# Kernel optimization log

Measured on AMD Instinct MI355X. Metric: run time of the kernel, lower is better.

The kernel has to match this reference:

```python
import jax, jax.numpy as jnp
import numpy as np

B, T = 128, 64          # batch, episode length
OB, AC, L, H = 32, 8, 128, 256  # ob_dim, ac_dim, latent_dim, mlp hidden
N_SUB = 4               # fixed Dopri5 substeps per interval (replaces adaptive PID controller)


def setup_inputs() -> dict:
    key = jax.random.key(0)
    ks = jax.random.split(key, 12)
    g = lambda k, shape, fan: jax.random.normal(k, shape, jnp.float32) / np.sqrt(fan)
    return {
        "ob": jax.random.normal(ks[0], (B, OB), jnp.float32),
        "acs": jax.random.normal(ks[1], (B, T, AC), jnp.float32),
        # strictly increasing timestamps (cumsum of uniform increments)
        "times": jnp.cumsum(jax.random.uniform(ks[2], (B, T), jnp.float32, 0.02, 0.1), axis=1),
        # ob encoder MLP (OB -> H -> L), relu hidden, identity out
        "We0": g(ks[3], (H, OB), OB), "be0": jnp.zeros((H,), jnp.float32),
        "We1": g(ks[4], (L, H), H), "be1": jnp.zeros((L,), jnp.float32),
        # latent dynamics MLP (L -> H -> H -> L)
        "Wd0": g(ks[5], (H, L), L), "bd0": jnp.zeros((H,), jnp.float32),
        "Wd1": g(ks[6], (H, H), H), "bd1": jnp.zeros((H,), jnp.float32),
        "Wd2": g(ks[7], (L, H), H), "bd2": jnp.zeros((L,), jnp.float32),
        # ob decoder MLP (L -> H -> OB)
        "Wo0": g(ks[8], (H, L), L), "bo0": jnp.zeros((H,), jnp.float32),
        "Wo1": g(ks[9], (OB, H), H), "bo1": jnp.zeros((OB,), jnp.float32),
        # GRU cell (input=AC, hidden=L), equinox layout: gates [r, z, n]
        "Wih": g(ks[10], (3 * L, AC), AC), "Whh": g(ks[11], (3 * L, L), L),
        "bih": jnp.zeros((3 * L,), jnp.float32), "bn": jnp.zeros((L,), jnp.float32),
    }


def reference(ob, acs, times, We0, be0, We1, be1, Wd0, bd0, Wd1, bd1, Wd2, bd2,
              Wo0, bo0, Wo1, bo1, Wih, Whh, bih, bn):
    def f(y):  # dynamics MLP on batched latent (B, L) -> (B, L)
        h1 = jax.nn.relu(y @ Wd0.T + bd0)
        h2 = jax.nn.relu(h1 @ Wd1.T + bd1)
        return h2 @ Wd2.T + bd2

    def gru(x, h):  # equinox GRUCell math, batched
        ir, iz, inn = jnp.split(x @ Wih.T + bih, 3, axis=-1)
        hr, hz, hn = jnp.split(h @ Whh.T, 3, axis=-1)
        r = jax.nn.sigmoid(ir + hr)
        z = jax.nn.sigmoid(iz + hz)
        n = jnp.tanh(inn + r * (hn + bn))
        return (1.0 - z) * n + z * h

    def dopri5_step(y, h):  # one Dopri5 (RK45) step, h: (B, 1) per-sample step size
        k1 = f(y)
        k2 = f(y + h * (0.2 * k1))
        k3 = f(y + h * (3/40 * k1 + 9/40 * k2))
        k4 = f(y + h * (44/45 * k1 - 56/15 * k2 + 32/9 * k3))
        k5 = f(y + h * (19372/6561 * k1 - 25360/2187 * k2 + 64448/6561 * k3 - 212/729 * k4))
        k6 = f(y + h * (9017/3168 * k1 - 355/33 * k2 + 46732/5247 * k3 + 49/176 * k4 - 5103/18656 * k5))
        return y + h * (35/384 * k1 + 500/1113 * k3 + 125/192 * k4 - 2187/6784 * k5 + 11/84 * k6)

    def integrate(y, dt):  # integrate latent ODE from 0 to dt with N_SUB fixed Dopri5 steps
        h = (dt / N_SUB)[:, None]
        return jax.lax.fori_loop(0, N_SUB, lambda i, yy: dopri5_step(yy, h), y)

    # encode first observation, consume first action
    latent0 = jax.nn.relu(ob @ We0.T + be0) @ We1.T + be1  # (B, L)
    latent0 = gru(acs[:, 0], latent0)

    dts = jnp.diff(times, axis=1)  # (B, T-1)

    def step(latent, xs):
        ac, dt = xs
        latent = integrate(latent, dt)
        latent = gru(ac, latent)
        return latent, latent

    xs = (jnp.swapaxes(acs[:, 1:], 0, 1), dts.T)  # time-major for scan
    _, lat_seq = jax.lax.scan(step, latent0, xs)  # (T-1, B, L)

    latents = jnp.concatenate([latent0[None], lat_seq], axis=0)  # (T, B, L)
    latents = jnp.swapaxes(latents, 0, 1)  # (B, T, L)

    h1 = jax.nn.relu(latents @ Wo0.T + bo0)
    return h1 @ Wo1.T + bo1  # (B, T, OB)
```

## Files before the change

### kernel.cpp

```cpp
#include <hip/hip_runtime.h>
#include <stdint.h>

#define NBATCH 128
#define NT     64
#define OBD    32
#define ACD    8
#define LDIM   128
#define HDIM   256

typedef _Float16 h2 __attribute__((ext_vector_type(2)));
typedef float    f4 __attribute__((ext_vector_type(4)));

#if defined(__has_builtin)
#  if __has_builtin(__builtin_amdgcn_fdot2)
#    define HAVE_FDOT2 1
#  endif
#endif

__device__ __forceinline__ float dot2f(h2 a, h2 b, float c) {
#ifdef HAVE_FDOT2
  return __builtin_amdgcn_fdot2(a, b, c, false);
#else
  return c + (float)a[0] * (float)b[0] + (float)a[1] * (float)b[1];
#endif
}

__device__ __forceinline__ h2 pkh(float a, float b) {
  h2 r; r[0] = (_Float16)a; r[1] = (_Float16)b; return r;
}

__device__ __forceinline__ h2 bch(float x) { return __builtin_bit_cast(h2, x); }
__device__ __forceinline__ float fch(h2 x) { return __builtin_bit_cast(float, x); }

__device__ __forceinline__ float sigmf(float x) { return 1.0f / (1.0f + expf(-x)); }

#define DOT4(W, I, Q) \
    a0 = dot2f(W[4*(I)+0], bch(Q.x), a0); \
    a1 = dot2f(W[4*(I)+1], bch(Q.y), a1); \
    a2 = dot2f(W[4*(I)+2], bch(Q.z), a2); \
    a3 = dot2f(W[4*(I)+3], bch(Q.w), a3);

#define PI(i) ((i) + (((i) >> 5) << 2))
#define PA(i) ((i) + (((i) >> 6) << 2))
#define PB(i) ((i) + (((i) >> 5) << 2))

__global__ void prep_w1(const float* __restrict__ Wd1, f4* __restrict__ ws4) {
  int idx = blockIdx.x * blockDim.x + threadIdx.x;
  int j  = idx >> 9;
  int tt = idx & 511;
  const float* src = Wd1 + (tt >> 1) * HDIM + (tt & 1) * 128 + j * 8;
  f4 c;
  c.x = fch(pkh(src[0], src[1]));
  c.y = fch(pkh(src[2], src[3]));
  c.z = fch(pkh(src[4], src[5]));
  c.w = fch(pkh(src[6], src[7]));
  ws4[j * 512 + tt] = c;
}

__global__ __attribute__((amdgpu_waves_per_eu(2, 2))) __launch_bounds__(512)
void ode_rnn_kernel(const float* __restrict__ ob,   const float* __restrict__ acs,
                    const float* __restrict__ times,
                    const float* __restrict__ We0,  const float* __restrict__ be0,
                    const float* __restrict__ We1,  const float* __restrict__ be1,
                    const float* __restrict__ Wd0,  const float* __restrict__ bd0,
                    const float* __restrict__ bd1,
                    const float* __restrict__ Wd2,  const float* __restrict__ bd2,
                    const float* __restrict__ Wo0,  const float* __restrict__ bo0,
                    const float* __restrict__ Wo1,  const float* __restrict__ bo1,
                    const float* __restrict__ Wih,  const float* __restrict__ Whh,
                    const float* __restrict__ bih,  const float* __restrict__ bn,
                    const f4* __restrict__ ws4,
                    float* __restrict__ out)
{
  const int t    = threadIdx.x;
  const int b    = blockIdx.x;
  const int p    = t >> 1;
  const int sub  = t & 1;
  const int r    = t >> 2;
  const int ksub = t & 3;

  __shared__ __align__(16) float s_lat[LDIM];
  __shared__ __align__(16) float s_gz[LDIM];
  __shared__ __align__(16) float s_gin[LDIM];
  __shared__ __align__(16) float s_ghn[LDIM];
  __shared__ __align__(16) float s_tmp[HDIM];
  __shared__ __align__(16) float s_obs[OBD];
  __shared__ __align__(16) float s_times[NT];
  __shared__ __align__(16) float s_acs[NT * ACD];
  __shared__ __align__(16) h2    s_in16[68];
  __shared__ __align__(16) h2    s_a16[132];
  __shared__ __align__(16) h2    s_b16[140];

  h2 w0[32], w2[32];
  {
    const float2* pp = (const float2*)(Wd0 + p * LDIM + sub * 64);
#pragma unroll
    for (int i = 0; i < 32; ++i) { float2 v = pp[i]; w0[i] = pkh(v.x, v.y); }
  }
  {
    const float2* pp = (const float2*)(Wd2 + r * HDIM + ksub * 64);
#pragma unroll
    for (int i = 0; i < 32; ++i) { float2 v = pp[i]; w2[i] = pkh(v.x, v.y); }
  }
  const f4* wsb = ws4 + t;

  const float bb0 = bd0[p];
  const float bb1 = bd1[p];
  const float bb2 = bd2[r];
  const float rb0 = bo0[p];
  const float gA  = (t < 3 * LDIM) ? bih[t] : 0.0f;
  const float bnr = (t < LDIM) ? bn[t] : 0.0f;

  float latr = 0.0f;

  auto substep = [&](float hs) {
    float k0 = 0, k1 = 0, k2 = 0, k3 = 0, k4 = 0;
#pragma unroll
    for (int s = 0; s < 6; ++s) {
      float a0, a1, a2, a3, v;
      f4 y0 = wsb[0 * 512], y1 = wsb[1 * 512];
      f4 y2 = wsb[2 * 512], y3 = wsb[3 * 512];
      a0 = a1 = a2 = a3 = 0.0f;
      {
        const f4* src = ((const f4*)s_in16) + sub * 9;
#pragma unroll
        for (int i = 0; i < 8; ++i) { f4 q = src[i]; DOT4(w0, i, q) }
      }
      v = (a0 + a1) + (a2 + a3);
      v += __shfl_xor(v, 1);
      v = fmaxf(v + bb0, 0.0f);
      { float ov = __shfl_xor(v, 2); if ((t & 3) == 0) s_a16[PA(t >> 2)] = pkh(v, ov); }
      __syncthreads();
      a0 = a1 = a2 = a3 = 0.0f;
      {
        const f4* act = ((const f4*)s_a16) + sub * 17;
        f4 q;
#define SDOT(WV, J) q = act[J]; \
        a0 = dot2f(bch(WV.x), bch(q.x), a0); \
        a1 = dot2f(bch(WV.y), bch(q.y), a1); \
        a2 = dot2f(bch(WV.z), bch(q.z), a2); \
        a3 = dot2f(bch(WV.w), bch(q.w), a3);
        f4 y4 = wsb[4 * 512],  y5 = wsb[5 * 512];
        SDOT(y0, 0)  SDOT(y1, 1)
        f4 y6 = wsb[6 * 512],  y7 = wsb[7 * 512];
        SDOT(y2, 2)  SDOT(y3, 3)
        f4 y8 = wsb[8 * 512],  y9 = wsb[9 * 512];
        SDOT(y4, 4)  SDOT(y5, 5)
        f4 y10 = wsb[10 * 512], y11 = wsb[11 * 512];
        SDOT(y6, 6)  SDOT(y7, 7)
        f4 y12 = wsb[12 * 512], y13 = wsb[13 * 512];
        SDOT(y8, 8)  SDOT(y9, 9)
        f4 y14 = wsb[14 * 512], y15 = wsb[15 * 512];
        SDOT(y10, 10) SDOT(y11, 11)
        SDOT(y12, 12) SDOT(y13, 13)
        SDOT(y14, 14) SDOT(y15, 15)
#undef SDOT
      }
      v = (a0 + a1) + (a2 + a3);
      v += __shfl_xor(v, 1);
      v = fmaxf(v + bb1, 0.0f);
      { float ov = __shfl_xor(v, 2); if ((t & 3) == 0) s_b16[PB(t >> 2)] = pkh(v, ov); }
      __syncthreads();
      a0 = a1 = a2 = a3 = 0.0f;
      {
        const f4* src = ((const f4*)s_b16) + ksub * 9;
#pragma unroll
        for (int i = 0; i < 8; ++i) { f4 q = src[i]; DOT4(w2, i, q) }
      }
      v = (a0 + a1) + (a2 + a3);
      v += __shfl_xor(v, 1);
      v += __shfl_xor(v, 2);
      float kv = v + bb2;
      float z;
      if (s == 0) {
        k0 = kv; z = latr + hs * (0.2f * kv);
      } else if (s == 1) {
        k1 = kv; z = latr + hs * ((3.0f/40.0f)*k0 + (9.0f/40.0f)*kv);
      } else if (s == 2) {
        k2 = kv; z = latr + hs * ((44.0f/45.0f)*k0 - (56.0f/15.0f)*k1
                                + (32.0f/9.0f)*kv);
      } else if (s == 3) {
        k3 = kv; z = latr + hs * ((19372.0f/6561.0f)*k0 - (25360.0f/2187.0f)*k1
                                + (64448.0f/6561.0f)*k2 - (212.0f/729.0f)*kv);
      } else if (s == 4) {
        k4 = kv; z = latr + hs * ((9017.0f/3168.0f)*k0 - (355.0f/33.0f)*k1
                                + (46732.0f/5247.0f)*k2 + (49.0f/176.0f)*k3
                                - (5103.0f/18656.0f)*kv);
      } else {
        z = latr + hs * ((35.0f/384.0f)*k0 + (500.0f/1113.0f)*k2
                       + (125.0f/192.0f)*k3 - (2187.0f/6784.0f)*k4
                       + (11.0f/84.0f)*kv);
        latr = z;
      }
      { float ov = __shfl_xor(z, 4); if ((t & 7) == 0) s_in16[PI(t >> 3)] = pkh(z, ov); }
      if (s == 5 && ksub == 0) s_lat[r] = z;
      __syncthreads();
    }
  };

  auto gru = [&](int ts) {
    __syncthreads();
    float vi = gA, vh = 0.0f;
    if (t < 3 * LDIM) {
      const float* xa = s_acs + ts * ACD;
      const f4* wiv = (const f4*)(Wih + t * ACD);
      f4 wa = wiv[0], wb = wiv[1];
      vi += wa.x*xa[0] + wa.y*xa[1] + wa.z*xa[2] + wa.w*xa[3]
          + wb.x*xa[4] + wb.y*xa[5] + wb.z*xa[6] + wb.w*xa[7];
      const f4* wh = (const f4*)(Whh + t * LDIM);
      const f4* xl = (const f4*)s_lat;
#pragma unroll
      for (int k2 = 0; k2 < LDIM / 4; ++k2) {
        f4 w = wh[k2], x = xl[k2];
        vh += w.x*x.x + w.y*x.y + w.z*x.z + w.w*x.w;
      }
    }
    if (t >= LDIM && t < 2 * LDIM)          s_gz[t - LDIM] = vi + vh;
    else if (t >= 2 * LDIM && t < 3 * LDIM) { s_gin[t - 2*LDIM] = vi; s_ghn[t - 2*LDIM] = vh; }
    __syncthreads();
    if (t < LDIM) {
      float rg = sigmf(vi + vh);
      float zg = sigmf(s_gz[t]);
      float ng = tanhf(s_gin[t] + rg * (s_ghn[t] + bnr));
      float y  = (1.0f - zg) * ng + zg * s_lat[t];
      s_lat[t] = y;
      float ov = __shfl_xor(y, 1);
      if (!(t & 1)) s_in16[PI(t >> 1)] = pkh(y, ov);
    }
  };

  auto decode = [&](int ts) {
    __syncthreads();
    latr = s_lat[r];
    float acc = 0.0f;
    {
      const f4* wr = (const f4*)(Wo0 + p * LDIM + sub * 64);
      const f4* xl = ((const f4*)s_lat) + sub * 16;
#pragma unroll
      for (int k2 = 0; k2 < 16; ++k2) {
        f4 w = wr[k2], x = xl[k2];
        acc += w.x*x.x + w.y*x.y + w.z*x.z + w.w*x.w;
      }
    }
    acc += __shfl_xor(acc, 1);
    acc = fmaxf(acc + rb0, 0.0f);
    { float ov = __shfl_xor(acc, 2); if ((t & 3) == 0) s_a16[PA(t >> 2)] = pkh(acc, ov); }
    __syncthreads();
    const int o  = t >> 4;
    const int sl = t & 15;
    float v2 = 0.0f;
    {
      const f4* wr = (const f4*)(Wo1 + o * HDIM + sl * 16);
      const h2* xs = s_a16 + sl * 8 + ((sl >> 3) << 2);
#pragma unroll
      for (int i = 0; i < 4; ++i) {
        f4 w = wr[i];
        h2 xa = xs[2*i], xb = xs[2*i+1];
        v2 += w.x*(float)xa[0] + w.y*(float)xa[1]
            + w.z*(float)xb[0] + w.w*(float)xb[1];
      }
    }
    v2 += __shfl_xor(v2, 1);
    v2 += __shfl_xor(v2, 2);
    v2 += __shfl_xor(v2, 4);
    v2 += __shfl_xor(v2, 8);
    if (sl == 0) out[((size_t)b * NT + ts) * OBD + o] = v2 + bo1[o];
    __syncthreads();
  };

  if (t < OBD) s_obs[t] = ob[b * OBD + t];
  if (t < NT)  s_times[t] = times[b * NT + t];
  s_acs[t] = acs[(size_t)b * NT * ACD + t];
  __syncthreads();
  if (t < HDIM) {
    float acc = be0[t];
    const float* wr = We0 + t * OBD;
#pragma unroll
    for (int j = 0; j < OBD; ++j) acc += wr[j] * s_obs[j];
    s_tmp[t] = fmaxf(acc, 0.0f);
  }
  __syncthreads();
  {
    const f4* wr = (const f4*)(We1 + r * HDIM + ksub * 64);
    const f4* xs = ((const f4*)s_tmp) + ksub * 16;
    float acc = 0.0f;
#pragma unroll
    for (int k = 0; k < 16; ++k) {
      f4 w = wr[k], x = xs[k];
      acc += w.x*x.x + w.y*x.y + w.z*x.z + w.w*x.w;
    }
    acc += __shfl_xor(acc, 1);
    acc += __shfl_xor(acc, 2);
    if (ksub == 0) s_lat[r] = acc + be1[r];
  }

  gru(0);
  decode(0);

#pragma unroll 1
  for (int ts = 1; ts < NT; ++ts) {
    float hs = 0.25f * (s_times[ts] - s_times[ts - 1]);
#pragma unroll 1
    for (int su = 0; su < 4; ++su) substep(hs);
    gru(ts);
    decode(ts);
  }
}

extern "C" void kernel_launch(void* const* d_in, const int* in_sizes, int n_in,
                              void* d_out, int out_size, void* d_ws, size_t ws_size,
                              hipStream_t stream) {
  (void)in_sizes; (void)n_in; (void)ws_size; (void)out_size;
  const float* ob    = (const float*)d_in[0];
  const float* acs   = (const float*)d_in[1];
  const float* times = (const float*)d_in[2];
  const float* We0   = (const float*)d_in[3];
  const float* be0   = (const float*)d_in[4];
  const float* We1   = (const float*)d_in[5];
  const float* be1   = (const float*)d_in[6];
  const float* Wd0   = (const float*)d_in[7];
  const float* bd0   = (const float*)d_in[8];
  const float* Wd1   = (const float*)d_in[9];
  const float* bd1   = (const float*)d_in[10];
  const float* Wd2   = (const float*)d_in[11];
  const float* bd2   = (const float*)d_in[12];
  const float* Wo0   = (const float*)d_in[13];
  const float* bo0   = (const float*)d_in[14];
  const float* Wo1   = (const float*)d_in[15];
  const float* bo1   = (const float*)d_in[16];
  const float* Wih   = (const float*)d_in[17];
  const float* Whh   = (const float*)d_in[18];
  const float* bih   = (const float*)d_in[19];
  const float* bn    = (const float*)d_in[20];

  f4* ws4 = (f4*)d_ws;

  prep_w1<<<dim3(16), dim3(512), 0, stream>>>(Wd1, ws4);
  ode_rnn_kernel<<<dim3(NBATCH), dim3(512), 0, stream>>>(
      ob, acs, times, We0, be0, We1, be1, Wd0, bd0, bd1, Wd2, bd2,
      Wo0, bo0, Wo1, bo1, Wih, Whh, bih, bn, ws4, (float*)d_out);
}
```

Before: 2.314 ms.

## Compute two output rows per thread group to halve shared-activation reads

Remaps the three dynamics-MLP matvecs so each thread group computes two adjacent output rows over a narrower K slice, reusing each shared-memory activation load for two weight rows. The Wd1 pre-pack layout, the register weight layouts for Wd0/Wd2, the shared buffer padding, and the Dopri5 stage math (now two latent rows per thread) are all changed to match. This is meant to cut LDS traffic and per-stage reduction overhead in the hot loop. In exchange it adds a shuffle level in each reduction, doubles the per-thread RK state registers, and changes the LDS bank-padding scheme.

```diff
diff --git a/kernel.cpp b/kernel.cpp
--- a/kernel.cpp
+++ b/kernel.cpp
@@ -34,21 +34,12 @@
 
 __device__ __forceinline__ float sigmf(float x) { return 1.0f / (1.0f + expf(-x)); }
 
-#define DOT4(W, I, Q) \
-    a0 = dot2f(W[4*(I)+0], bch(Q.x), a0); \
-    a1 = dot2f(W[4*(I)+1], bch(Q.y), a1); \
-    a2 = dot2f(W[4*(I)+2], bch(Q.z), a2); \
-    a3 = dot2f(W[4*(I)+3], bch(Q.w), a3);
-
-#define PI(i) ((i) + (((i) >> 5) << 2))
-#define PA(i) ((i) + (((i) >> 6) << 2))
-#define PB(i) ((i) + (((i) >> 5) << 2))
-
 __global__ void prep_w1(const float* __restrict__ Wd1, f4* __restrict__ ws4) {
   int idx = blockIdx.x * blockDim.x + threadIdx.x;
   int j  = idx >> 9;
   int tt = idx & 511;
-  const float* src = Wd1 + (tt >> 1) * HDIM + (tt & 1) * 128 + j * 8;
+  const float* src = Wd1 + (2 * (tt >> 2) + (j & 1)) * HDIM
+                         + (tt & 3) * 64 + (j >> 1) * 8;
   f4 c;
   c.x = fch(pkh(src[0], src[1]));
   c.y = fch(pkh(src[2], src[3]));
@@ -72,12 +63,12 @@
                     const f4* __restrict__ ws4,
                     float* __restrict__ out)
 {
-  const int t    = threadIdx.x;
-  const int b    = blockIdx.x;
-  const int p    = t >> 1;
-  const int sub  = t & 1;
-  const int r    = t >> 2;
-  const int ksub = t & 3;
+  const int t  = threadIdx.x;
+  const int b  = blockIdx.x;
+  const int G1 = t >> 2, K1 = t & 3;
+  const int G3 = t >> 3, K3 = t & 7;
+  const int p   = t >> 1;
+  const int sub = t & 1;
 
   __shared__ __align__(16) float s_lat[LDIM];
   __shared__ __align__(16) float s_gz[LDIM];
@@ -87,113 +78,165 @@
   __shared__ __align__(16) float s_obs[OBD];
   __shared__ __align__(16) float s_times[NT];
   __shared__ __align__(16) float s_acs[NT * ACD];
-  __shared__ __align__(16) h2    s_in16[68];
-  __shared__ __align__(16) h2    s_a16[132];
-  __shared__ __align__(16) h2    s_b16[140];
+  __shared__ __align__(16) h2    s_in16[96];
+  __shared__ __align__(16) h2    s_a16[152];
+  __shared__ __align__(16) h2    s_b16[160];
 
   h2 w0[32], w2[32];
   {
-    const float2* pp = (const float2*)(Wd0 + p * LDIM + sub * 64);
-#pragma unroll
-    for (int i = 0; i < 32; ++i) { float2 v = pp[i]; w0[i] = pkh(v.x, v.y); }
+    const float2* r0 = (const float2*)(Wd0 + (2 * G1) * LDIM + K1 * 32);
+    const float2* r1 = (const float2*)(Wd0 + (2 * G1 + 1) * LDIM + K1 * 32);
+#pragma unroll
+    for (int i = 0; i < 16; ++i) {
+      float2 u = r0[i], v = r1[i];
+      w0[i] = pkh(u.x, u.y); w0[16 + i] = pkh(v.x, v.y);
+    }
   }
   {
-    const float2* pp = (const float2*)(Wd2 + r * HDIM + ksub * 64);
-#pragma unroll
-    for (int i = 0; i < 32; ++i) { float2 v = pp[i]; w2[i] = pkh(v.x, v.y); }
+    const float2* r0 = (const float2*)(Wd2 + (2 * G3) * HDIM + K3 * 32);
+    const float2* r1 = (const float2*)(Wd2 + (2 * G3 + 1) * HDIM + K3 * 32);
+#pragma unroll
+    for (int i = 0; i < 16; ++i) {
+      float2 u = r0[i], v = r1[i];
+      w2[i] = pkh(u.x, u.y); w2[16 + i] = pkh(v.x, v.y);
+    }
   }
   const f4* wsb = ws4 + t;
 
-  const float bb0 = bd0[p];
-  const float bb1 = bd1[p];
-  const float bb2 = bd2[r];
-  const float rb0 = bo0[p];
-  const float gA  = (t < 3 * LDIM) ? bih[t] : 0.0f;
-  const float bnr = (t < LDIM) ? bn[t] : 0.0f;
-
-  float latr = 0.0f;
+  const float bb00 = bd0[2 * G1], bb01 = bd0[2 * G1 + 1];
+  const float bb10 = bd1[2 * G1], bb11 = bd1[2 * G1 + 1];
+  const float bb20 = bd2[2 * G3], bb21 = bd2[2 * G3 + 1];
+  const float rb0  = bo0[p];
+  const float gA   = (t < 3 * LDIM) ? bih[t] : 0.0f;
+  const float bnr  = (t < LDIM) ? bn[t] : 0.0f;
+
+  float latr0 = 0.0f, latr1 = 0.0f;
 
   auto substep = [&](float hs) {
-    float k0 = 0, k1 = 0, k2 = 0, k3 = 0, k4 = 0;
+    float k00 = 0, k10 = 0, k20 = 0, k30 = 0, k40 = 0;
+    float k01 = 0, k11 = 0, k21 = 0, k31 = 0, k41 = 0;
 #pragma unroll
     for (int s = 0; s < 6; ++s) {
-      float a0, a1, a2, a3, v;
       f4 y0 = wsb[0 * 512], y1 = wsb[1 * 512];
       f4 y2 = wsb[2 * 512], y3 = wsb[3 * 512];
-      a0 = a1 = a2 = a3 = 0.0f;
+      float a0, a1, b0, b1, v0, v1;
+      a0 = a1 = b0 = b1 = 0.0f;
       {
-        const f4* src = ((const f4*)s_in16) + sub * 9;
-#pragma unroll
-        for (int i = 0; i < 8; ++i) { f4 q = src[i]; DOT4(w0, i, q) }
-      }
-      v = (a0 + a1) + (a2 + a3);
-      v += __shfl_xor(v, 1);
-      v = fmaxf(v + bb0, 0.0f);
-      { float ov = __shfl_xor(v, 2); if ((t & 3) == 0) s_a16[PA(t >> 2)] = pkh(v, ov); }
+        const f4* act = ((const f4*)s_in16) + K1 * 6;
+#pragma unroll
+        for (int i = 0; i < 4; ++i) {
+          f4 q = act[i];
+          a0 = dot2f(w0[4*i+0], bch(q.x), a0);
+          a1 = dot2f(w0[4*i+1], bch(q.y), a1);
+          a0 = dot2f(w0[4*i+2], bch(q.z), a0);
+          a1 = dot2f(w0[4*i+3], bch(q.w), a1);
+          b0 = dot2f(w0[16+4*i+0], bch(q.x), b0);
+          b1 = dot2f(w0[16+4*i+1], bch(q.y), b1);
+          b0 = dot2f(w0[16+4*i+2], bch(q.z), b0);
+          b1 = dot2f(w0[16+4*i+3], bch(q.w), b1);
+        }
+      }
+      v0 = a0 + a1; v1 = b0 + b1;
+      v0 += __shfl_xor(v0, 1); v0 += __shfl_xor(v0, 2);
+      v1 += __shfl_xor(v1, 1); v1 += __shfl_xor(v1, 2);
+      v0 = fmaxf(v0 + bb00, 0.0f); v1 = fmaxf(v1 + bb01, 0.0f);
+      if (K1 == 0) s_a16[(G1 >> 5) * 40 + (G1 & 31)] = pkh(v0, v1);
       __syncthreads();
-      a0 = a1 = a2 = a3 = 0.0f;
+      a0 = a1 = b0 = b1 = 0.0f;
       {
-        const f4* act = ((const f4*)s_a16) + sub * 17;
+        const f4* act = ((const f4*)s_a16) + K1 * 10;
         f4 q;
-#define SDOT(WV, J) q = act[J]; \
-        a0 = dot2f(bch(WV.x), bch(q.x), a0); \
-        a1 = dot2f(bch(WV.y), bch(q.y), a1); \
-        a2 = dot2f(bch(WV.z), bch(q.z), a2); \
-        a3 = dot2f(bch(WV.w), bch(q.w), a3);
+#define SD2(W0V, W1V, J) q = act[J]; \
+        a0 = dot2f(bch(W0V.x), bch(q.x), a0); \
+        a1 = dot2f(bch(W0V.y), bch(q.y), a1); \
+        a0 = dot2f(bch(W0V.z), bch(q.z), a0); \
+        a1 = dot2f(bch(W0V.w), bch(q.w), a1); \
+        b0 = dot2f(bch(W1V.x), bch(q.x), b0); \
+        b1 = dot2f(bch(W1V.y), bch(q.y), b1); \
+        b0 = dot2f(bch(W1V.z), bch(q.z), b0); \
+        b1 = dot2f(bch(W1V.w), bch(q.w), b1);
         f4 y4 = wsb[4 * 512],  y5 = wsb[5 * 512];
-        SDOT(y0, 0)  SDOT(y1, 1)
+        SD2(y0, y1, 0)
         f4 y6 = wsb[6 * 512],  y7 = wsb[7 * 512];
-        SDOT(y2, 2)  SDOT(y3, 3)
+        SD2(y2, y3, 1)
         f4 y8 = wsb[8 * 512],  y9 = wsb[9 * 512];
-        SDOT(y4, 4)  SDOT(y5, 5)
+        SD2(y4, y5, 2)
         f4 y10 = wsb[10 * 512], y11 = wsb[11 * 512];
-        SDOT(y6, 6)  SDOT(y7, 7)
+        SD2(y6, y7, 3)
         f4 y12 = wsb[12 * 512], y13 = wsb[13 * 512];
-        SDOT(y8, 8)  SDOT(y9, 9)
+        SD2(y8, y9, 4)
         f4 y14 = wsb[14 * 512], y15 = wsb[15 * 512];
-        SDOT(y10, 10) SDOT(y11, 11)
-        SDOT(y12, 12) SDOT(y13, 13)
-        SDOT(y14, 14) SDOT(y15, 15)
-#undef SDOT
-      }
-      v = (a0 + a1) + (a2 + a3);
-      v += __shfl_xor(v, 1);
-      v = fmaxf(v + bb1, 0.0f);
-      { float ov = __shfl_xor(v, 2); if ((t & 3) == 0) s_b16[PB(t >> 2)] = pkh(v, ov); }
+        SD2(y10, y11, 5)
+        SD2(y12, y13, 6)
+        SD2(y14, y15, 7)
+#undef SD2
+      }
+      v0 = a0 + a1; v1 = b0 + b1;
+      v0 += __shfl_xor(v0, 1); v0 += __shfl_xor(v0, 2);
+      v1 += __shfl_xor(v1, 1); v1 += __shfl_xor(v1, 2);
+      v0 = fmaxf(v0 + bb10, 0.0f); v1 = fmaxf(v1 + bb11, 0.0f);
+      if (K1 == 0) s_b16[(G1 >> 4) * 20 + (G1 & 15)] = pkh(v0, v1);
       __syncthreads();
-      a0 = a1 = a2 = a3 = 0.0f;
+      a0 = a1 = b0 = b1 = 0.0f;
       {
-        const f4* src = ((const f4*)s_b16) + ksub * 9;
-#pragma unroll
-        for (int i = 0; i < 8; ++i) { f4 q = src[i]; DOT4(w2, i, q) }
-      }
-      v = (a0 + a1) + (a2 + a3);
-      v += __shfl_xor(v, 1);
-      v += __shfl_xor(v, 2);
-      float kv = v + bb2;
-      float z;
+        const f4* act = ((const f4*)s_b16) + K3 * 5;
+#pragma unroll
+        for (int i = 0; i < 4; ++i) {
+          f4 q = act[i];
+          a0 = dot2f(w2[4*i+0], bch(q.x), a0);
+          a1 = dot2f(w2[4*i+1], bch(q.y), a1);
+          a0 = dot2f(w2[4*i+2], bch(q.z), a0);
+          a1 = dot2f(w2[4*i+3], bch(q.w), a1);
+          b0 = dot2f(w2[16+4*i+0], bch(q.x), b0);
+          b1 = dot2f(w2[16+4*i+1], bch(q.y), b1);
+          b0 = dot2f(w2[16+4*i+2], bch(q.z), b0);
+          b1 = dot2f(w2[16+4*i+3], bch(q.w), b1);
+        }
+      }
+      v0 = a0 + a1; v1 = b0 + b1;
+      v0 += __shfl_xor(v0, 1); v0 += __shfl_xor(v0, 2); v0 += __shfl_xor(v0, 4);
+      v1 += __shfl_xor(v1, 1); v1 += __shfl_xor(v1, 2); v1 += __shfl_xor(v1, 4);
+      float kv0 = v0 + bb20, kv1 = v1 + bb21;
+      float z0, z1;
       if (s == 0) {
-        k0 = kv; z = latr + hs * (0.2f * kv);
+        k00 = kv0; k01 = kv1;
+        z0 = latr0 + hs * (0.2f * kv0);
+        z1 = latr1 + hs * (0.2f * kv1);
       } else if (s == 1) {
-        k1 = kv; z = latr + hs * ((3.0f/40.0f)*k0 + (9.0f/40.0f)*kv);
+        k10 = kv0; k11 = kv1;
+        z0 = latr0 + hs * ((3.0f/40.0f)*k00 + (9.0f/40.0f)*kv0);
+        z1 = latr1 + hs * ((3.0f/40.0f)*k01 + (9.0f/40.0f)*kv1);
       } else if (s == 2) {
-        k2 = kv; z = latr + hs * ((44.0f/45.0f)*k0 - (56.0f/15.0f)*k1
-                                + (32.0f/9.0f)*kv);
+        k20 = kv0; k21 = kv1;
+        z0 = latr0 + hs * ((44.0f/45.0f)*k00 - (56.0f/15.0f)*k10 + (32.0f/9.0f)*kv0);
+        z1 = latr1 + hs * ((44.0f/45.0f)*k01 - (56.0f/15.0f)*k11 + (32.0f/9.0f)*kv1);
       } else if (s == 3) {
-        k3 = kv; z = latr + hs * ((19372.0f/6561.0f)*k0 - (25360.0f/2187.0f)*k1
-                                + (64448.0f/6561.0f)*k2 - (212.0f/729.0f)*kv);
+        k30 = kv0; k31 = kv1;
+        z0 = latr0 + hs * ((19372.0f/6561.0f)*k00 - (25360.0f/2187.0f)*k10
+                         + (64448.0f/6561.0f)*k20 - (212.0f/729.0f)*kv0);
+        z1 = latr1 + hs * ((19372.0f/6561.0f)*k01 - (25360.0f/2187.0f)*k11
+                         + (64448.0f/6561.0f)*k21 - (212.0f/729.0f)*kv1);
       } else if (s == 4) {
-        k4 = kv; z = latr + hs * ((9017.0f/3168.0f)*k0 - (355.0f/33.0f)*k1
-                                + (46732.0f/5247.0f)*k2 + (49.0f/176.0f)*k3
-                                - (5103.0f/18656.0f)*kv);
+        k40 = kv0; k41 = kv1;
+        z0 = latr0 + hs * ((9017.0f/3168.0f)*k00 - (355.0f/33.0f)*k10
+                         + (46732.0f/5247.0f)*k20 + (49.0f/176.0f)*k30
+                         - (5103.0f/18656.0f)*kv0);
+        z1 = latr1 + hs * ((9017.0f/3168.0f)*k01 - (355.0f/33.0f)*k11
+                         + (46732.0f/5247.0f)*k21 + (49.0f/176.0f)*k31
+                         - (5103.0f/18656.0f)*kv1);
       } else {
-        z = latr + hs * ((35.0f/384.0f)*k0 + (500.0f/1113.0f)*k2
-                       + (125.0f/192.0f)*k3 - (2187.0f/6784.0f)*k4
-                       + (11.0f/84.0f)*kv);
-        latr = z;
-      }
-      { float ov = __shfl_xor(z, 4); if ((t & 7) == 0) s_in16[PI(t >> 3)] = pkh(z, ov); }
-      if (s == 5 && ksub == 0) s_lat[r] = z;
+        z0 = latr0 + hs * ((35.0f/384.0f)*k00 + (500.0f/1113.0f)*k20
+                         + (125.0f/192.0f)*k30 - (2187.0f/6784.0f)*k40
+                         + (11.0f/84.0f)*kv0);
+        z1 = latr1 + hs * ((35.0f/384.0f)*k01 + (500.0f/1113.0f)*k21
+                         + (125.0f/192.0f)*k31 - (2187.0f/6784.0f)*k41
+                         + (11.0f/84.0f)*kv1);
+        latr0 = z0; latr1 = z1;
+      }
+      if (K3 == 0) {
+        s_in16[(G3 >> 4) * 24 + (G3 & 15)] = pkh(z0, z1);
+        if (s == 5) { s_lat[2*G3] = z0; s_lat[2*G3 + 1] = z1; }
+      }
       __syncthreads();
     }
   };
@@ -225,13 +268,16 @@
       float y  = (1.0f - zg) * ng + zg * s_lat[t];
       s_lat[t] = y;
       float ov = __shfl_xor(y, 1);
-      if (!(t & 1)) s_in16[PI(t >> 1)] = pkh(y, ov);
+      if (!(t & 1)) {
+        int g = t >> 1;
+        s_in16[(g >> 4) * 24 + (g & 15)] = pkh(y, ov);
+      }
     }
   };
 
   auto decode = [&](int ts) {
     __syncthreads();
-    latr = s_lat[r];
+    { float2 ld = *(const float2*)(s_lat + 2 * G3); latr0 = ld.x; latr1 = ld.y; }
     float acc = 0.0f;
     {
       const f4* wr = (const f4*)(Wo0 + p * LDIM + sub * 64);
@@ -244,7 +290,8 @@
     }
     acc += __shfl_xor(acc, 1);
     acc = fmaxf(acc + rb0, 0.0f);
-    { float ov = __shfl_xor(acc, 2); if ((t & 3) == 0) s_a16[PA(t >> 2)] = pkh(acc, ov); }
+    { float ov = __shfl_xor(acc, 2);
+      if ((t & 3) == 0) { int i = t >> 2; s_a16[i + ((i >> 6) << 2)] = pkh(acc, ov); } }
     __syncthreads();
     const int o  = t >> 4;
     const int sl = t & 15;
@@ -281,8 +328,9 @@
   }
   __syncthreads();
   {
-    const f4* wr = (const f4*)(We1 + r * HDIM + ksub * 64);
-    const f4* xs = ((const f4*)s_tmp) + ksub * 16;
+    const int rr = t >> 2, kk = t & 3;
+    const f4* wr = (const f4*)(We1 + rr * HDIM + kk * 64);
+    const f4* xs = ((const f4*)s_tmp) + kk * 16;
     float acc = 0.0f;
 #pragma unroll
     for (int k = 0; k < 16; ++k) {
@@ -291,7 +339,7 @@
     }
     acc += __shfl_xor(acc, 1);
     acc += __shfl_xor(acc, 2);
-    if (ksub == 0) s_lat[r] = acc + be1[r];
+    if (kk == 0) s_lat[rr] = acc + be1[rr];
   }
 
   gru(0);
```

After: 2.368 ms. 1.02x slower.
